# Kernel tuning notes

Measured on AMD Instinct MI355X. Metric: run time of the kernel, lower is better.

## Reference

```python
import jax, jax.numpy as jnp
import numpy as np

N_NODES = 10000
N_EDGES = 640000
D_IN = 128
D_INTER = 128


def gcn_conv(x, edge_index, edge_weight, W, b):
    # PyG GCNConv: out = D^{-1/2} (A + I) D^{-1/2} (X W) + b
    n = x.shape[0]
    h = x @ W  # [N, D_out]
    row, col = edge_index[0], edge_index[1]  # source, target
    loop = jnp.arange(n, dtype=row.dtype)
    row = jnp.concatenate([row, loop])
    col = jnp.concatenate([col, loop])
    ew = jnp.concatenate([edge_weight, jnp.ones((n,), edge_weight.dtype)])
    deg = jax.ops.segment_sum(ew, col, num_segments=n)  # in-degree incl. self loops
    dinv = jnp.where(deg > 0, jax.lax.rsqrt(deg), jnp.zeros_like(deg))
    norm = dinv[row] * ew * dinv[col]  # [E+N]
    msgs = norm[:, None] * h[row]  # gather + scale
    out = jax.ops.segment_sum(msgs, col, num_segments=n)  # scatter-add aggregate
    return out + b


def setup_inputs() -> dict:
    key = jax.random.key(0)
    ks = jax.random.split(key, 8)
    x = jax.random.normal(ks[0], (N_NODES, D_IN), dtype=jnp.float32)
    edge_index = jax.random.randint(ks[1], (2, N_EDGES), 0, N_NODES, dtype=jnp.int64)
    edge_weight = jax.random.uniform(ks[2], (N_EDGES,), dtype=jnp.float32)
    # Glorot-ish init for linear weights, zeros for bias (PyG default)
    s1 = 1.0 / np.sqrt(D_IN)
    s2 = 1.0 / np.sqrt(D_INTER)
    W1 = jax.random.uniform(ks[3], (D_IN, D_INTER), jnp.float32, -s1, s1)
    b1 = jnp.zeros((D_INTER,), jnp.float32)
    W2 = jax.random.uniform(ks[4], (D_INTER, D_IN), jnp.float32, -s2, s2)
    b2 = jnp.zeros((D_IN,), jnp.float32)
    return {"x": x, "edge_index": edge_index, "edge_weight": edge_weight,
            "W1": W1, "b1": b1, "W2": W2, "b2": b2}


def reference(x, edge_index, edge_weight, W1, b1, W2, b2):
    # GCN.forward in eval mode: dropout is identity
    h = jax.nn.relu(gcn_conv(x, edge_index, edge_weight, W1, b1))
    out = jax.nn.relu(gcn_conv(h, edge_index, edge_weight, W2, b2))
    return out
```

## Files before the change

kernel.cpp:

```cpp
#include <hip/hip_runtime.h>

#define NN 10000
#define NE 640000
#define D  128
#define SEG 32
#define PAD_SHIFT 8
#define GEMM_BLOCKS ((NN + 31) / 32)
#define CSTRIDE 10240
#define COUNT_BLOCKS (NE / 1024)

__device__ __forceinline__ int xcc_id() {
    unsigned x;
    asm volatile("s_getreg_b32 %0, hwreg(HW_REG_XCC_ID)" : "=s"(x));
    return (int)(x & 7);
}


__global__ __launch_bounds__(256) void zero_kernel(int* __restrict__ p, int n) {
    int i = blockIdx.x * 256 + threadIdx.x;
    if (i < n) p[i] = 0;
}


__global__ __launch_bounds__(256) void fused_gemm_cs_kernel(const float* __restrict__ X,
                                                            const float* __restrict__ W,
                                                            float* __restrict__ H,
                                                            const int* __restrict__ ei,
                                                            const float* __restrict__ ew,
                                                            int* __restrict__ cnt8,
                                                            int2* __restrict__ epack) {
    int bid = blockIdx.x;
    if (bid < GEMM_BLOCKS) {
        __shared__ float xs[32][D];
        int t  = threadIdx.x;
        int d  = t & 127;
        int rh = t >> 7;
        int r0 = bid * 32;
#pragma unroll
        for (int r = 0; r < 16; ++r) {
            int rr = r0 + rh * 16 + r;
            xs[rh * 16 + r][d] = (rr < NN) ? X[(size_t)rr * D + d] : 0.0f;
        }
        __syncthreads();
        float acc[16];
#pragma unroll
        for (int r = 0; r < 16; ++r) acc[r] = 0.0f;
        for (int k = 0; k < D; k += 4) {
            float w0 = W[(k + 0) * D + d];
            float w1 = W[(k + 1) * D + d];
            float w2 = W[(k + 2) * D + d];
            float w3 = W[(k + 3) * D + d];
#pragma unroll
            for (int r = 0; r < 16; ++r) {
                float4 xv = *reinterpret_cast<const float4*>(&xs[rh * 16 + r][k]);
                acc[r] = fmaf(xv.x, w0, acc[r]);
                acc[r] = fmaf(xv.y, w1, acc[r]);
                acc[r] = fmaf(xv.z, w2, acc[r]);
                acc[r] = fmaf(xv.w, w3, acc[r]);
            }
        }
#pragma unroll
        for (int r = 0; r < 16; ++r) {
            int rr = r0 + rh * 16 + r;
            if (rr < NN) H[(size_t)rr * D + d] = acc[r];
        }
    } else {
        int e0 = (bid - GEMM_BLOCKS) * 1024 + threadIdx.x;
        int x  = xcc_id();
        int* mycnt = cnt8 + x * CSTRIDE;
        int   c[4], s[4];
        float w[4];
#pragma unroll
        for (int k = 0; k < 4; ++k) {
            int e = e0 + k * 256;
            c[k] = ei[NE + e];
            s[k] = ei[e];
            w[k] = ew[e];
        }
        int lr[4];
#pragma unroll
        for (int k = 0; k < 4; ++k) lr[k] = atomicAdd(&mycnt[c[k]], 1);
#pragma unroll
        for (int k = 0; k < 4; ++k) {
            if (lr[k] < SEG) {
                int2 v;
                v.x = s[k];
                v.y = __float_as_int(w[k]);
                epack[((size_t)c[k] << PAD_SHIFT) + x * SEG + lr[k]] = v;
            }
        }
    }
}


__global__ __launch_bounds__(256) void degdinv_kernel(const int* __restrict__ cnt8,
                                                      const int2* __restrict__ epack,
                                                      float* __restrict__ dinv) {
    int node = blockIdx.x * 4 + (threadIdx.x >> 6);
    if (node >= NN) return;
    int lane = threadIdx.x & 63;
    const int2* base = epack + ((size_t)node << PAD_SHIFT);
    float s = 0.0f;
#pragma unroll
    for (int x = 0; x < 8; ++x) {
        int mx = cnt8[x * CSTRIDE + node];
        if (lane < mx) s += __int_as_float(base[x * SEG + lane].y);
    }
#pragma unroll
    for (int off = 32; off; off >>= 1) s += __shfl_down(s, off);
    if (lane == 0) dinv[node] = rsqrtf(s + 1.0f);
}


__global__ __launch_bounds__(256) void gemm_kernel(const float* __restrict__ X,
                                                   const float* __restrict__ W,
                                                   float* __restrict__ H) {
    __shared__ float xs[32][D];
    int t  = threadIdx.x;
    int d  = t & 127;
    int rh = t >> 7;
    int r0 = blockIdx.x * 32;
#pragma unroll
    for (int r = 0; r < 16; ++r) {
        int rr = r0 + rh * 16 + r;
        xs[rh * 16 + r][d] = (rr < NN) ? X[(size_t)rr * D + d] : 0.0f;
    }
    __syncthreads();
    float acc[16];
#pragma unroll
    for (int r = 0; r < 16; ++r) acc[r] = 0.0f;
    for (int k = 0; k < D; k += 4) {
        float w0 = W[(k + 0) * D + d];
        float w1 = W[(k + 1) * D + d];
        float w2 = W[(k + 2) * D + d];
        float w3 = W[(k + 3) * D + d];
#pragma unroll
        for (int r = 0; r < 16; ++r) {
            float4 xv = *reinterpret_cast<const float4*>(&xs[rh * 16 + r][k]);
            acc[r] = fmaf(xv.x, w0, acc[r]);
            acc[r] = fmaf(xv.y, w1, acc[r]);
            acc[r] = fmaf(xv.z, w2, acc[r]);
            acc[r] = fmaf(xv.w, w3, acc[r]);
        }
    }
#pragma unroll
    for (int r = 0; r < 16; ++r) {
        int rr = r0 + rh * 16 + r;
        if (rr < NN) H[(size_t)rr * D + d] = acc[r];
    }
}


__global__ __launch_bounds__(64) void agg_half_kernel(const float* __restrict__ H,
                                                      const int* __restrict__ cnt8,
                                                      const int2* __restrict__ epack,
                                                      const float* __restrict__ dinv,
                                                      const float* __restrict__ bias,
                                                      float* __restrict__ out) {
    __shared__ int   s_src[256];
    __shared__ float s_n[256];
    int i    = blockIdx.x;
    int slot = i & 7;
    int hh   = slot & 1;
    int c    = (i >> 3) * 4 + (slot >> 1);
    int t    = threadIdx.x;
    int d    = (hh << 6) | t;
    const int2* eb = epack + ((size_t)c << PAD_SHIFT);
    float di = dinv[c];
    int tot = 0;
#pragma unroll
    for (int x = 0; x < 8; ++x) {
        int mx = cnt8[x * CSTRIDE + c];
        if (t < mx) {
            int2 v = eb[x * SEG + t];
            s_src[tot + t] = v.x;
            s_n[tot + t]   = dinv[v.x] * __int_as_float(v.y);
        }
        tot += mx;
    }
    __syncthreads();
    int m = tot;
    float acc = di * H[(size_t)c * D + d];
    int jj = 0;
    for (; jj + 8 <= m; jj += 8) {
#pragma unroll
        for (int k = 0; k < 8; ++k)
            acc = fmaf(s_n[jj + k], H[(size_t)s_src[jj + k] * D + d], acc);
    }
    for (; jj < m; ++jj)
        acc = fmaf(s_n[jj], H[(size_t)s_src[jj] * D + d], acc);
    out[(size_t)c * D + d] = fmaxf(fmaf(di, acc, bias[d]), 0.0f);
}


extern "C" void kernel_launch(void* const* d_in, const int* in_sizes, int n_in,
                              void* d_out, int out_size, void* d_ws, size_t ws_size,
                              hipStream_t stream) {
    const float* x  = (const float*)d_in[0];
    const int*   ei = (const int*)  d_in[1];
    const float* ew = (const float*)d_in[2];
    const float* W1 = (const float*)d_in[3];
    const float* b1 = (const float*)d_in[4];
    const float* W2 = (const float*)d_in[5];
    const float* b2 = (const float*)d_in[6];
    float* out = (float*)d_out;

    char* ws = (char*)d_ws;
    size_t off = 0;
    auto alloc = [&](size_t bytes) {
        void* p = ws + off;
        off = (off + bytes + 255) & ~(size_t)255;
        return p;
    };
    int*   cnt8  = (int*)  alloc(8 * CSTRIDE * 4);
    float* dinv  = (float*)alloc(NN * 4);
    int2*  epack = (int2*) alloc(((size_t)NN << PAD_SHIFT) * 8);
    float* h     = (float*)alloc((size_t)NN * D * 4);
    float* g     = (float*)alloc((size_t)NN * D * 4);

    zero_kernel<<<(8 * CSTRIDE + 255) / 256, 256, 0, stream>>>(cnt8, 8 * CSTRIDE);
    fused_gemm_cs_kernel<<<GEMM_BLOCKS + COUNT_BLOCKS, 256, 0, stream>>>(
        x, W1, h, ei, ew, cnt8, epack);
    degdinv_kernel<<<(NN + 3) / 4, 256, 0, stream>>>(cnt8, epack, dinv);

    agg_half_kernel<<<NN * 2, 64, 0, stream>>>(h, cnt8, epack, dinv, b1, g);
    gemm_kernel    <<<(NN + 31) / 32, 256, 0, stream>>>(g, W2, h);
    agg_half_kernel<<<NN * 2, 64, 0, stream>>>(h, cnt8, epack, dinv, b2, out);
}
```

Measured before the change: 156.2 us.

## Fuse all GCN stages into one cooperative persistent kernel with grid syncs

Replaces the six separate kernel launches with a single cooperative kernel that runs the zeroing, CSR build plus first GEMM, degree normalization, two aggregations and second GEMM as phases separated by grid-wide barriers. The intent is to remove per-launch overhead and inter-kernel gaps. Aggregation is restructured to have each 256-thread block process four nodes per iteration in a grid-stride loop, with block barriers between iterations. A non-cooperative fallback path with equivalent grid-stride kernels is kept; the fixed grid size reduces parallelism for the irregular aggregation phases and adds grid-sync costs.

```diff
diff --git a/kernel.cpp b/kernel.cpp
--- a/kernel.cpp
+++ b/kernel.cpp
@@ -1,13 +1,17 @@
 #include <hip/hip_runtime.h>
+#include <hip/hip_cooperative_groups.h>
+
+namespace cg = cooperative_groups;
 
 #define NN 10000
 #define NE 640000
 #define D  128
 #define SEG 32
 #define PAD_SHIFT 8
-#define GEMM_BLOCKS ((NN + 31) / 32)
 #define CSTRIDE 10240
-#define COUNT_BLOCKS (NE / 1024)
+#define GEMM_TILES 313
+#define NCHUNK 625
+#define COOP_GRID 1024
 
 __device__ __forceinline__ int xcc_id() {
     unsigned x;
@@ -15,111 +19,13 @@
     return (int)(x & 7);
 }
 
-
-__global__ __launch_bounds__(256) void zero_kernel(int* __restrict__ p, int n) {
-    int i = blockIdx.x * 256 + threadIdx.x;
-    if (i < n) p[i] = 0;
-}
-
-
-__global__ __launch_bounds__(256) void fused_gemm_cs_kernel(const float* __restrict__ X,
-                                                            const float* __restrict__ W,
-                                                            float* __restrict__ H,
-                                                            const int* __restrict__ ei,
-                                                            const float* __restrict__ ew,
-                                                            int* __restrict__ cnt8,
-                                                            int2* __restrict__ epack) {
-    int bid = blockIdx.x;
-    if (bid < GEMM_BLOCKS) {
-        __shared__ float xs[32][D];
-        int t  = threadIdx.x;
-        int d  = t & 127;
-        int rh = t >> 7;
-        int r0 = bid * 32;
-#pragma unroll
-        for (int r = 0; r < 16; ++r) {
-            int rr = r0 + rh * 16 + r;
-            xs[rh * 16 + r][d] = (rr < NN) ? X[(size_t)rr * D + d] : 0.0f;
-        }
-        __syncthreads();
-        float acc[16];
-#pragma unroll
-        for (int r = 0; r < 16; ++r) acc[r] = 0.0f;
-        for (int k = 0; k < D; k += 4) {
-            float w0 = W[(k + 0) * D + d];
-            float w1 = W[(k + 1) * D + d];
-            float w2 = W[(k + 2) * D + d];
-            float w3 = W[(k + 3) * D + d];
-#pragma unroll
-            for (int r = 0; r < 16; ++r) {
-                float4 xv = *reinterpret_cast<const float4*>(&xs[rh * 16 + r][k]);
-                acc[r] = fmaf(xv.x, w0, acc[r]);
-                acc[r] = fmaf(xv.y, w1, acc[r]);
-                acc[r] = fmaf(xv.z, w2, acc[r]);
-                acc[r] = fmaf(xv.w, w3, acc[r]);
-            }
-        }
-#pragma unroll
-        for (int r = 0; r < 16; ++r) {
-            int rr = r0 + rh * 16 + r;
-            if (rr < NN) H[(size_t)rr * D + d] = acc[r];
-        }
-    } else {
-        int e0 = (bid - GEMM_BLOCKS) * 1024 + threadIdx.x;
-        int x  = xcc_id();
-        int* mycnt = cnt8 + x * CSTRIDE;
-        int   c[4], s[4];
-        float w[4];
-#pragma unroll
-        for (int k = 0; k < 4; ++k) {
-            int e = e0 + k * 256;
-            c[k] = ei[NE + e];
-            s[k] = ei[e];
-            w[k] = ew[e];
-        }
-        int lr[4];
-#pragma unroll
-        for (int k = 0; k < 4; ++k) lr[k] = atomicAdd(&mycnt[c[k]], 1);
-#pragma unroll
-        for (int k = 0; k < 4; ++k) {
-            if (lr[k] < SEG) {
-                int2 v;
-                v.x = s[k];
-                v.y = __float_as_int(w[k]);
-                epack[((size_t)c[k] << PAD_SHIFT) + x * SEG + lr[k]] = v;
-            }
-        }
-    }
-}
-
-
-__global__ __launch_bounds__(256) void degdinv_kernel(const int* __restrict__ cnt8,
-                                                      const int2* __restrict__ epack,
-                                                      float* __restrict__ dinv) {
-    int node = blockIdx.x * 4 + (threadIdx.x >> 6);
-    if (node >= NN) return;
-    int lane = threadIdx.x & 63;
-    const int2* base = epack + ((size_t)node << PAD_SHIFT);
-    float s = 0.0f;
-#pragma unroll
-    for (int x = 0; x < 8; ++x) {
-        int mx = cnt8[x * CSTRIDE + node];
-        if (lane < mx) s += __int_as_float(base[x * SEG + lane].y);
-    }
-#pragma unroll
-    for (int off = 32; off; off >>= 1) s += __shfl_down(s, off);
-    if (lane == 0) dinv[node] = rsqrtf(s + 1.0f);
-}
-
-
-__global__ __launch_bounds__(256) void gemm_kernel(const float* __restrict__ X,
-                                                   const float* __restrict__ W,
-                                                   float* __restrict__ H) {
-    __shared__ float xs[32][D];
-    int t  = threadIdx.x;
+__device__ __forceinline__ void gemm_tile(const float* __restrict__ X,
+                                          const float* __restrict__ W,
+                                          float* __restrict__ H,
+                                          int tile, int t, float (*xs)[D]) {
     int d  = t & 127;
     int rh = t >> 7;
-    int r0 = blockIdx.x * 32;
+    int r0 = tile * 32;
 #pragma unroll
     for (int r = 0; r < 16; ++r) {
         int rr = r0 + rh * 16 + r;
@@ -148,48 +54,189 @@
         int rr = r0 + rh * 16 + r;
         if (rr < NN) H[(size_t)rr * D + d] = acc[r];
     }
-}
-
-
-__global__ __launch_bounds__(64) void agg_half_kernel(const float* __restrict__ H,
-                                                      const int* __restrict__ cnt8,
-                                                      const int2* __restrict__ epack,
-                                                      const float* __restrict__ dinv,
-                                                      const float* __restrict__ bias,
-                                                      float* __restrict__ out) {
-    __shared__ int   s_src[256];
-    __shared__ float s_n[256];
-    int i    = blockIdx.x;
-    int slot = i & 7;
-    int hh   = slot & 1;
-    int c    = (i >> 3) * 4 + (slot >> 1);
-    int t    = threadIdx.x;
-    int d    = (hh << 6) | t;
-    const int2* eb = epack + ((size_t)c << PAD_SHIFT);
-    float di = dinv[c];
-    int tot = 0;
-#pragma unroll
-    for (int x = 0; x < 8; ++x) {
-        int mx = cnt8[x * CSTRIDE + c];
-        if (t < mx) {
-            int2 v = eb[x * SEG + t];
-            s_src[tot + t] = v.x;
-            s_n[tot + t]   = dinv[v.x] * __int_as_float(v.y);
-        }
-        tot += mx;
-    }
     __syncthreads();
-    int m = tot;
-    float acc = di * H[(size_t)c * D + d];
-    int jj = 0;
-    for (; jj + 8 <= m; jj += 8) {
-#pragma unroll
-        for (int k = 0; k < 8; ++k)
-            acc = fmaf(s_n[jj + k], H[(size_t)s_src[jj + k] * D + d], acc);
-    }
-    for (; jj < m; ++jj)
-        acc = fmaf(s_n[jj], H[(size_t)s_src[jj] * D + d], acc);
-    out[(size_t)c * D + d] = fmaxf(fmaf(di, acc, bias[d]), 0.0f);
+}
+
+__device__ __forceinline__ void phase_zero(int bid, int t, int grid,
+                                           int* __restrict__ cnt8) {
+    for (int i = bid * 256 + t; i < 8 * CSTRIDE; i += grid * 256) cnt8[i] = 0;
+}
+
+__device__ __forceinline__ void phase_build(int bid, int t, int grid,
+                                            const float* __restrict__ X,
+                                            const float* __restrict__ W1,
+                                            float* __restrict__ H,
+                                            const int* __restrict__ ei,
+                                            const float* __restrict__ ew,
+                                            int* __restrict__ cnt8,
+                                            int2* __restrict__ epack,
+                                            float (*xs)[D]) {
+    if (bid < GEMM_TILES) {
+        gemm_tile(X, W1, H, bid, t, xs);
+    } else {
+        int nb = grid - GEMM_TILES;
+        for (int chunk = bid - GEMM_TILES; chunk < NCHUNK; chunk += nb) {
+            int e0 = chunk * 1024 + t;
+            int x  = xcc_id();
+            int* mycnt = cnt8 + x * CSTRIDE;
+            int   c[4], sR[4];
+            float w[4];
+#pragma unroll
+            for (int k = 0; k < 4; ++k) {
+                int e = e0 + k * 256;
+                c[k]  = ei[NE + e];
+                sR[k] = ei[e];
+                w[k]  = ew[e];
+            }
+            int lr[4];
+#pragma unroll
+            for (int k = 0; k < 4; ++k) lr[k] = atomicAdd(&mycnt[c[k]], 1);
+#pragma unroll
+            for (int k = 0; k < 4; ++k) {
+                if (lr[k] < SEG) {
+                    int2 v;
+                    v.x = sR[k];
+                    v.y = __float_as_int(w[k]);
+                    epack[((size_t)c[k] << PAD_SHIFT) + x * SEG + lr[k]] = v;
+                }
+            }
+        }
+    }
+}
+
+__device__ __forceinline__ void phase_deg(int bid, int t, int grid,
+                                          const int* __restrict__ cnt8,
+                                          const int2* __restrict__ epack,
+                                          float* __restrict__ dinv) {
+    int lane = t & 63;
+    for (int node = bid * 4 + (t >> 6); node < NN; node += grid * 4) {
+        int mxv = (lane < 8) ? min(cnt8[lane * CSTRIDE + node], SEG) : 0;
+        const int2* eb = epack + ((size_t)node << PAD_SHIFT);
+        float s = 0.0f;
+#pragma unroll
+        for (int x = 0; x < 8; ++x) {
+            int mxx = __shfl(mxv, x);
+            if (lane < mxx) s += __int_as_float(eb[x * SEG + lane].y);
+        }
+#pragma unroll
+        for (int off = 32; off; off >>= 1) s += __shfl_down(s, off);
+        if (lane == 0) dinv[node] = rsqrtf(s + 1.0f);
+    }
+}
+
+__device__ __forceinline__ void phase_agg(int bid, int t, int grid,
+                                          const float* __restrict__ Hsrc,
+                                          const int* __restrict__ cnt8,
+                                          const int2* __restrict__ epack,
+                                          const float* __restrict__ dinv,
+                                          const float* __restrict__ bias,
+                                          float* __restrict__ outp,
+                                          float (*xs)[D]) {
+    int p    = bid & 1;
+    int r    = bid >> 1;
+    int half = grid >> 1;
+    int gg   = t >> 6;
+    int lane = t & 63;
+    int d    = (p << 6) | lane;
+    int*   s_src = ((int*)xs) + gg * 256;
+    float* s_n   = ((float*)xs) + 1024 + gg * 256;
+    float bd = bias[d];
+    for (int cbase = r * 4; cbase < NN; cbase += half * 4) {
+        int c = cbase + gg;
+        bool act = (c < NN);
+        int tot = 0;
+        float di = 0.0f;
+        if (act) {
+            int mxv = (lane < 8) ? min(cnt8[lane * CSTRIDE + c], SEG) : 0;
+            const int2* eb = epack + ((size_t)c << PAD_SHIFT);
+            int mx[8], pre[8];
+#pragma unroll
+            for (int x = 0; x < 8; ++x) { mx[x] = __shfl(mxv, x); pre[x] = tot; tot += mx[x]; }
+#pragma unroll
+            for (int x = 0; x < 8; ++x) {
+                if (lane < mx[x]) {
+                    int2 v = eb[x * SEG + lane];
+                    int pp = pre[x] + lane;
+                    s_src[pp] = v.x;
+                    s_n[pp]   = dinv[v.x] * __int_as_float(v.y);
+                }
+            }
+            di = dinv[c];
+        }
+        __syncthreads();
+        if (act) {
+            float acc = di * Hsrc[(size_t)c * D + d];
+            int jj = 0;
+            for (; jj + 8 <= tot; jj += 8) {
+#pragma unroll
+                for (int k = 0; k < 8; ++k)
+                    acc = fmaf(s_n[jj + k], Hsrc[(size_t)s_src[jj + k] * D + d], acc);
+            }
+            for (; jj < tot; ++jj)
+                acc = fmaf(s_n[jj], Hsrc[(size_t)s_src[jj] * D + d], acc);
+            outp[(size_t)c * D + d] = fmaxf(fmaf(di, acc, bd), 0.0f);
+        }
+        __syncthreads();
+    }
+}
+
+
+__global__ __launch_bounds__(256, 4) void mega_kernel(const float* __restrict__ X,
+                                                      const int* __restrict__ ei,
+                                                      const float* __restrict__ ew,
+                                                      const float* __restrict__ W1,
+                                                      const float* __restrict__ b1,
+                                                      const float* __restrict__ W2,
+                                                      const float* __restrict__ b2,
+                                                      float* __restrict__ out,
+                                                      int* __restrict__ cnt8,
+                                                      float* __restrict__ dinv,
+                                                      int2* __restrict__ epack,
+                                                      float* __restrict__ h,
+                                                      float* __restrict__ g) {
+    cg::grid_group grid = cg::this_grid();
+    __shared__ float xs[32][D];
+    int bid = blockIdx.x, t = threadIdx.x, gs = gridDim.x;
+
+    phase_zero(bid, t, gs, cnt8);
+    __threadfence(); grid.sync();
+    phase_build(bid, t, gs, X, W1, h, ei, ew, cnt8, epack, xs);
+    __threadfence(); grid.sync();
+    phase_deg(bid, t, gs, cnt8, epack, dinv);
+    __threadfence(); grid.sync();
+    phase_agg(bid, t, gs, h, cnt8, epack, dinv, b1, g, xs);
+    __threadfence(); grid.sync();
+    if (bid < GEMM_TILES) gemm_tile(g, W2, h, bid, t, xs);
+    __threadfence(); grid.sync();
+    phase_agg(bid, t, gs, h, cnt8, epack, dinv, b2, out, xs);
+}
+
+
+__global__ __launch_bounds__(256) void k_zero(int* cnt8) {
+    phase_zero(blockIdx.x, threadIdx.x, gridDim.x, cnt8);
+}
+__global__ __launch_bounds__(256, 4) void k_build(const float* X, const float* W1,
+                                                  float* H, const int* ei,
+                                                  const float* ew, int* cnt8,
+                                                  int2* epack) {
+    __shared__ float xs[32][D];
+    phase_build(blockIdx.x, threadIdx.x, gridDim.x, X, W1, H, ei, ew, cnt8, epack, xs);
+}
+__global__ __launch_bounds__(256) void k_deg(const int* cnt8, const int2* epack,
+                                             float* dinv) {
+    phase_deg(blockIdx.x, threadIdx.x, gridDim.x, cnt8, epack, dinv);
+}
+__global__ __launch_bounds__(256, 4) void k_agg(const float* Hsrc, const int* cnt8,
+                                                const int2* epack, const float* dinv,
+                                                const float* bias, float* outp) {
+    __shared__ float xs[32][D];
+    phase_agg(blockIdx.x, threadIdx.x, gridDim.x, Hsrc, cnt8, epack, dinv, bias, outp, xs);
+}
+__global__ __launch_bounds__(256, 4) void k_gemm(const float* X, const float* W,
+                                                 float* H) {
+    __shared__ float xs[32][D];
+    for (int tile = blockIdx.x; tile < GEMM_TILES; tile += gridDim.x)
+        gemm_tile(X, W, H, tile, threadIdx.x, xs);
 }
 
 
@@ -218,12 +265,23 @@
     float* h     = (float*)alloc((size_t)NN * D * 4);
     float* g     = (float*)alloc((size_t)NN * D * 4);
 
-    zero_kernel<<<(8 * CSTRIDE + 255) / 256, 256, 0, stream>>>(cnt8, 8 * CSTRIDE);
-    fused_gemm_cs_kernel<<<GEMM_BLOCKS + COUNT_BLOCKS, 256, 0, stream>>>(
-        x, W1, h, ei, ew, cnt8, epack);
-    degdinv_kernel<<<(NN + 3) / 4, 256, 0, stream>>>(cnt8, epack, dinv);
-
-    agg_half_kernel<<<NN * 2, 64, 0, stream>>>(h, cnt8, epack, dinv, b1, g);
-    gemm_kernel    <<<(NN + 31) / 32, 256, 0, stream>>>(g, W2, h);
-    agg_half_kernel<<<NN * 2, 64, 0, stream>>>(h, cnt8, epack, dinv, b2, out);
-}
+    int maxPerCU = 0;
+    hipError_t oe = hipOccupancyMaxActiveBlocksPerMultiprocessor(&maxPerCU,
+                                                                 mega_kernel, 256, 0);
+    bool coop = (oe == hipSuccess) && (maxPerCU * 256 >= COOP_GRID);
+    if (coop) {
+        void* args[] = {(void*)&x, (void*)&ei, (void*)&ew, (void*)&W1, (void*)&b1,
+                        (void*)&W2, (void*)&b2, (void*)&out, (void*)&cnt8,
+                        (void*)&dinv, (void*)&epack, (void*)&h, (void*)&g};
+        hipError_t le = hipLaunchCooperativeKernel((const void*)mega_kernel,
+                                                   dim3(COOP_GRID), dim3(256),
+                                                   args, 0, stream);
+        if (le == hipSuccess) return;
+    }
+    k_zero <<<320, 256, 0, stream>>>(cnt8);
+    k_build<<<GEMM_TILES + NCHUNK, 256, 0, stream>>>(x, W1, h, ei, ew, cnt8, epack);
+    k_deg  <<<2500, 256, 0, stream>>>(cnt8, epack, dinv);
+    k_agg  <<<5000, 256, 0, stream>>>(h, cnt8, epack, dinv, b1, g);
+    k_gemm <<<GEMM_TILES, 256, 0, stream>>>(g, W2, h);
+    k_agg  <<<5000, 256, 0, stream>>>(h, cnt8, epack, dinv, b2, out);
+}
```

Result: faster. 153.1 us (-2.0%).
